# Performance work log

Hardware: AMD Instinct MI355X
Metric: run time of the kernel (lower is better)

Reference implementation:

```python
import jax, jax.numpy as jnp
import numpy as np

D_MODEL, N_HEADS, D_HEAD = 1024, 16, 64
IGNORE = -1e5

def setup_inputs() -> dict:
    key = jax.random.key(0)
    ks = jax.random.split(key, 5)
    std = 0.02
    return {
        "resid_pre": jax.random.normal(ks[0], (4, 2048, D_MODEL), dtype=jnp.float32),
        "W_Q": jax.random.normal(ks[1], (N_HEADS, D_MODEL, D_HEAD), dtype=jnp.float32) * std,
        "W_K": jax.random.normal(ks[2], (N_HEADS, D_MODEL, D_HEAD), dtype=jnp.float32) * std,
        "W_V": jax.random.normal(ks[3], (N_HEADS, D_MODEL, D_HEAD), dtype=jnp.float32) * std,
        "W_O": jax.random.normal(ks[4], (N_HEADS, D_HEAD, D_MODEL), dtype=jnp.float32) * std,
        "b_Q": jnp.zeros((N_HEADS, D_HEAD), dtype=jnp.float32),
        "b_K": jnp.zeros((N_HEADS, D_HEAD), dtype=jnp.float32),
        "b_V": jnp.zeros((N_HEADS, D_HEAD), dtype=jnp.float32),
        "b_O": jnp.zeros((D_MODEL,), dtype=jnp.float32),
    }

def reference(resid_pre, W_Q, W_K, W_V, W_O, b_Q, b_K, b_V, b_O):
    # q/k/v: [batch, posn, n_heads, d_head]
    q = jnp.einsum("hmd,bsm->bshd", W_Q, resid_pre) + b_Q
    k = jnp.einsum("hmd,bsm->bshd", W_K, resid_pre) + b_K
    v = jnp.einsum("hmd,bsm->bshd", W_V, resid_pre) + b_V
    # scores: [batch, n_heads, posn_q, posn_k]
    scores = jnp.einsum("bqhd,bkhd->bhqk", q, k) / jnp.sqrt(jnp.float32(D_HEAD))
    S = resid_pre.shape[1]
    causal = jnp.tril(jnp.ones((S, S), dtype=bool))  # keep where True
    scores = jnp.where(causal, scores, jnp.float32(IGNORE))
    probs = jax.nn.softmax(scores, axis=-1)
    z = jnp.einsum("bhqk,bkhd->bqhd", probs, v)  # [batch, posn_q, n_heads, d_head]
    # project each head to d_model and sum over heads, then add b_O
    attn_out = jnp.einsum("hdm,bqhd->bqm", W_O, z) + b_O
    return attn_out
```

## Files before the change

kernel.cpp:

```cpp
#include <hip/hip_runtime.h>

typedef __bf16 bf16;
typedef __attribute__((ext_vector_type(8))) __bf16 bf16x8;
typedef __attribute__((ext_vector_type(4))) float f32x4;

__device__ __forceinline__ void gload_lds16(const void* g, void* l) {
  __builtin_amdgcn_global_load_lds(
      (const __attribute__((address_space(1))) unsigned int*)(g),
      (__attribute__((address_space(3))) unsigned int*)(l),
      16, 0, 0);
}

__device__ __forceinline__ float exp2_hw(float x) {
  float r; asm("v_exp_f32 %0, %1" : "=v"(r) : "v"(x)); return r;
}
__device__ __forceinline__ unsigned cvtpk_bf16(float a, float b) {
  unsigned r; asm("v_cvt_pk_bf16_f32 %0, %1, %2" : "=v"(r) : "v"(a), "v"(b)); return r;
}

#define QSCALE 0.1803368867f

__global__ __launch_bounds__(256) void pack_all(const float* __restrict__ x,
                                                const float* __restrict__ WQ, const float* __restrict__ WK,
                                                const float* __restrict__ WV,
                                                const float* __restrict__ bQ, const float* __restrict__ bK,
                                                const float* __restrict__ bV,
                                                bf16* __restrict__ Xb, bf16* __restrict__ Wt,
                                                float* __restrict__ biaso) {
  __shared__ float tile[64][65];
  int bid = blockIdx.x;
  int t = threadIdx.x;
  if (bid < 4096) {
    int i = (bid * 256 + t) * 8;
    float4 a = *(const float4*)(x + i);
    float4 b = *(const float4*)(x + i + 4);
    bf16x8 v;
    v[0] = (bf16)a.x; v[1] = (bf16)a.y; v[2] = (bf16)a.z; v[3] = (bf16)a.w;
    v[4] = (bf16)b.x; v[5] = (bf16)b.y; v[6] = (bf16)b.z; v[7] = (bf16)b.w;
    *(bf16x8*)(Xb + i) = v;
  } else if (bid < 4864) {
    int wb = bid - 4096;
    int p = wb >> 8, h = (wb >> 4) & 15, k0 = (wb & 15) * 64;
    const float* src = (p == 0 ? WQ : p == 1 ? WK : WV) + h * 65536;
    float scl = (p == 0) ? QSCALE : 1.0f;
    int c = t & 63, r4 = t >> 6;
#pragma unroll
    for (int rr = 0; rr < 16; ++rr) {
      int k = r4 + rr * 4;
      tile[k][c] = src[(k0 + k) * 64 + c];
    }
    __syncthreads();
#pragma unroll
    for (int rr = 0; rr < 16; ++rr) {
      int d = r4 + rr * 4;
      Wt[(p * 1024 + h * 64 + d) * 1024 + k0 + c] = (bf16)(tile[c][d] * scl);
    }
  } else {
    int i = (bid - 4864) * 256 + t;
    if (i < 3072) {
      int p = i >> 10, j = i & 1023;
      float v = (p == 0 ? bQ : p == 1 ? bK : bV)[j];
      biaso[i] = (p == 0) ? v * QSCALE : v;
    }
  }
}

__global__ __launch_bounds__(256) void pack_wo(const float* __restrict__ WO, bf16* __restrict__ Wt) {
  int bid = blockIdx.x;
  int r0 = (bid >> 4) * 64, c0 = (bid & 15) * 64;
  __shared__ float tile[64][65];
  int t = threadIdx.x, c = t & 63, r4 = t >> 6;
#pragma unroll
  for (int rr = 0; rr < 16; ++rr) {
    int r = r4 + rr * 4;
    tile[r][c] = WO[(r0 + r) * 1024 + c0 + c];
  }
  __syncthreads();
#pragma unroll
  for (int rr = 0; rr < 16; ++rr) {
    int m = r4 + rr * 4;
    Wt[(c0 + m) * 1024 + r0 + c] = (bf16)tile[c][m];
  }
}

template <int OUTF32>
__global__ __launch_bounds__(512, 2) void gemm_bt(const bf16* __restrict__ A, const bf16* __restrict__ Bt,
                                                  const float* __restrict__ bias, void* __restrict__ Cv,
                                                  int M, int N, int K) {
  __shared__ bf16 As[256 * 64];
  __shared__ bf16 Bs[128 * 64];
  int tid = threadIdx.x;
  int wv = tid >> 6, ln = tid & 63, lr = ln & 15, lh = ln >> 4;
  int wr = wv >> 1, wc = wv & 1;
  int row0 = blockIdx.y * 256, col0 = blockIdx.x * 128;
  int ss = (ln & 7) ^ (ln >> 3);
  const char* ga = (const char*)(A + (long)(row0 + wv * 32 + (ln >> 3)) * K) + ss * 16;
  const char* gb = (const char*)(Bt + (long)(col0 + wv * 16 + (ln >> 3)) * K) + ss * 16;
  long rowskip = (long)8 * K * 2;
  f32x4 acc[4][4] = {};
  for (int k0 = 0; k0 < K; k0 += 64) {
#pragma unroll
    for (int i = 0; i < 4; ++i)
      gload_lds16(ga + (long)k0 * 2 + i * rowskip, (char*)As + (wv * 32 + i * 8) * 128);
#pragma unroll
    for (int i = 0; i < 2; ++i)
      gload_lds16(gb + (long)k0 * 2 + i * rowskip, (char*)Bs + (wv * 16 + i * 8) * 128);
    __syncthreads();
    bf16x8 af[4][2], bfr[4][2];
#pragma unroll
    for (int mi = 0; mi < 4; ++mi)
#pragma unroll
      for (int ks = 0; ks < 2; ++ks) {
        int row = wr * 64 + mi * 16 + lr;
        int o = row * 128 + (((ks * 4 + lh) ^ (row & 7)) << 4);
        af[mi][ks] = *(const bf16x8*)((const char*)As + o);
      }
#pragma unroll
    for (int ni = 0; ni < 4; ++ni)
#pragma unroll
      for (int ks = 0; ks < 2; ++ks) {
        int row = wc * 64 + ni * 16 + lr;
        int o = row * 128 + (((ks * 4 + lh) ^ (row & 7)) << 4);
        bfr[ni][ks] = *(const bf16x8*)((const char*)Bs + o);
      }
    __builtin_amdgcn_s_setprio(1);
#pragma unroll
    for (int ks = 0; ks < 2; ++ks)
#pragma unroll
      for (int mi = 0; mi < 4; ++mi)
#pragma unroll
        for (int ni = 0; ni < 4; ++ni)
          acc[mi][ni] = __builtin_amdgcn_mfma_f32_16x16x32_bf16(af[mi][ks], bfr[ni][ks], acc[mi][ni], 0, 0, 0);
    __builtin_amdgcn_s_setprio(0);
    __syncthreads();
  }
#pragma unroll
  for (int mi = 0; mi < 4; ++mi) {
    int row = row0 + wr * 64 + mi * 16 + lh * 4;
#pragma unroll
    for (int ni = 0; ni < 4; ++ni) {
      int col = col0 + wc * 64 + ni * 16 + lr;
      float bvv = bias[col];
#pragma unroll
      for (int r = 0; r < 4; ++r) {
        float v = acc[mi][ni][r] + bvv;
        if (OUTF32) ((float*)Cv)[(long)(row + r) * N + col] = v;
        else        ((bf16*)Cv)[(long)(row + r) * N + col] = (bf16)v;
      }
    }
  }
}

__global__ __launch_bounds__(256, 2) void flash(const bf16* __restrict__ Qkv, bf16* __restrict__ Z) {
  __shared__ bf16 Vt[2][64 * 64];
  __shared__ unsigned char Pl[4][4096];
  const float MASKV = -144269.5041f;
  int bid = blockIdx.x;
  int pair = bid >> 6;
  int bh = (bid & 7) * 8 + ((bid >> 3) & 7);
  int b = bh >> 4, h = bh & 15;
  int tid = threadIdx.x;
  int wv = tid >> 6, ln = tid & 63, lr = ln & 15, lh = ln >> 4;
  const bf16* Qg = Qkv + (long)b * 2048 * 3072 + h * 64;
  const bf16* Kg = Qg + 1024;
  const bf16* Vg = Qg + 2048;
  int vs0 = (tid >> 3) * 2, vd0 = (tid & 7) * 8;
  char* pw = (char*)Pl[wv];

  bf16x8 v0, v1;
  auto loadV = [&](int kvrow0) {
    v0 = *(const bf16x8*)(Vg + (long)(kvrow0 + vs0) * 3072 + vd0);
    v1 = *(const bf16x8*)(Vg + (long)(kvrow0 + vs0 + 1) * 3072 + vd0);
  };
  auto writeV = [&](bf16* vd) {
#pragma unroll
    for (int j = 0; j < 8; ++j) {
      int d = vd0 + j;
      int o = (d * 128 + vs0 * 2) ^ ((((d & 7) ^ (d >> 3)) & 7) << 4);
      unsigned int pk = (unsigned int)__builtin_bit_cast(unsigned short, (bf16)v0[j])
                      | ((unsigned int)__builtin_bit_cast(unsigned short, (bf16)v1[j]) << 16);
      *(unsigned int*)((char*)vd + o) = pk;
    }
  };

#pragma unroll 1
  for (int half = 0; half < 2; ++half) {
    int qt = half ? 15 - pair : pair;
    int q0 = qt * 128;
    int nt = 2 * (qt + 1);
    loadV(0);
    bf16x8 bq[2][2];
#pragma unroll
    for (int mi = 0; mi < 2; ++mi)
#pragma unroll
      for (int ks = 0; ks < 2; ++ks)
        bq[mi][ks] = *(const bf16x8*)(Qg + (long)(q0 + wv * 32 + mi * 16 + lr) * 3072 + ks * 32 + lh * 8);
    writeV(Vt[0]);
    __syncthreads();

    f32x4 oa[4][2] = {};
    float m_st[2], l_st[2];
    m_st[0] = m_st[1] = -1e30f;
    l_st[0] = l_st[1] = 0.f;

    int cur = 0;
    for (int t = 0; t < nt; ++t) {
      int kv0 = t * 64;
      bool more = (t + 1 < nt);
      bf16x8 kf[4][2];
#pragma unroll
      for (int n = 0; n < 4; ++n)
#pragma unroll
        for (int ks = 0; ks < 2; ++ks)
          kf[n][ks] = *(const bf16x8*)(Kg + (long)(kv0 + n * 16 + lr) * 3072 + ks * 32 + lh * 8);
      if (more) loadV(kv0 + 64);
      f32x4 sc[2][4];
      __builtin_amdgcn_s_setprio(1);
#pragma unroll
      for (int mi = 0; mi < 2; ++mi)
#pragma unroll
        for (int n = 0; n < 4; ++n) {
          f32x4 zacc = {0.f, 0.f, 0.f, 0.f};
          zacc = __builtin_amdgcn_mfma_f32_16x16x32_bf16(kf[n][0], bq[mi][0], zacc, 0, 0, 0);
          zacc = __builtin_amdgcn_mfma_f32_16x16x32_bf16(kf[n][1], bq[mi][1], zacc, 0, 0, 0);
          sc[mi][n] = zacc;
        }
      __builtin_amdgcn_s_setprio(0);
      if (kv0 + 63 > q0) {
#pragma unroll
        for (int mi = 0; mi < 2; ++mi) {
          int qrow = q0 + wv * 32 + mi * 16 + lr;
#pragma unroll
          for (int n = 0; n < 4; ++n) {
            int kvb = kv0 + n * 16 + lh * 4;
#pragma unroll
            for (int r = 0; r < 4; ++r)
              if (kvb + r > qrow) sc[mi][n][r] = MASKV;
          }
        }
      }
#pragma unroll
      for (int mi = 0; mi < 2; ++mi) {
        float mx = sc[mi][0][0];
#pragma unroll
        for (int n = 0; n < 4; ++n)
#pragma unroll
          for (int r = 0; r < 4; ++r) mx = fmaxf(mx, sc[mi][n][r]);
        mx = fmaxf(mx, __shfl_xor(mx, 16));
        mx = fmaxf(mx, __shfl_xor(mx, 32));
        if (!__all(mx <= m_st[mi] + 8.0f)) {
          float mn = fmaxf(m_st[mi], mx);
          float resc = exp2_hw(m_st[mi] - mn);
          m_st[mi] = mn;
          l_st[mi] *= resc;
#pragma unroll
          for (int n2 = 0; n2 < 4; ++n2)
#pragma unroll
            for (int r = 0; r < 4; ++r) oa[n2][mi][r] *= resc;
        }
        float s = 0.f;
#pragma unroll
        for (int n = 0; n < 4; ++n)
#pragma unroll
          for (int r = 0; r < 4; ++r) {
            float p = exp2_hw(sc[mi][n][r] - m_st[mi]);
            sc[mi][n][r] = p;
            s += p;
          }
        s += __shfl_xor(s, 16);
        s += __shfl_xor(s, 32);
        l_st[mi] += s;
      }
#pragma unroll
      for (int mi = 0; mi < 2; ++mi) {
        int row = mi * 16 + lr;
#pragma unroll
        for (int n = 0; n < 4; ++n) {
          int addr = row * 128 + ((n * 32 + lh * 8) ^ ((row & 7) << 4));
          uint2 val = { cvtpk_bf16(sc[mi][n][0], sc[mi][n][1]),
                        cvtpk_bf16(sc[mi][n][2], sc[mi][n][3]) };
          *(uint2*)(pw + addr) = val;
        }
      }
      if (more) writeV(Vt[cur ^ 1]);
      bf16x8 pa[2][2];
#pragma unroll
      for (int mi = 0; mi < 2; ++mi)
#pragma unroll
        for (int ks = 0; ks < 2; ++ks) {
          int row = mi * 16 + lr;
          int o = row * 128 + (((ks * 4 + lh) ^ (row & 7)) << 4);
          pa[mi][ks] = *(const bf16x8*)(pw + o);
        }
      __builtin_amdgcn_s_setprio(1);
#pragma unroll
      for (int n2 = 0; n2 < 4; ++n2) {
        int row = n2 * 16 + lr;
        int o0 = row * 128 + ((((0 + lh) ^ (row & 7) ^ ((row >> 3) & 7)) & 7) << 4);
        int o1 = row * 128 + ((((4 + lh) ^ (row & 7) ^ ((row >> 3) & 7)) & 7) << 4);
        bf16x8 vf0 = *(const bf16x8*)((const char*)Vt[cur] + o0);
        bf16x8 vf1 = *(const bf16x8*)((const char*)Vt[cur] + o1);
#pragma unroll
        for (int mi = 0; mi < 2; ++mi) {
          oa[n2][mi] = __builtin_amdgcn_mfma_f32_16x16x32_bf16(vf0, pa[mi][0], oa[n2][mi], 0, 0, 0);
          oa[n2][mi] = __builtin_amdgcn_mfma_f32_16x16x32_bf16(vf1, pa[mi][1], oa[n2][mi], 0, 0, 0);
        }
      }
      __builtin_amdgcn_s_setprio(0);
      __syncthreads();
      cur ^= 1;
    }
#pragma unroll
    for (int mi = 0; mi < 2; ++mi) {
      float inv = 1.0f / l_st[mi];
      int q = q0 + wv * 32 + mi * 16 + lr;
      bf16* zb = Z + ((long)b * 2048 + q) * 1024 + h * 64 + lh * 4;
#pragma unroll
      for (int n2 = 0; n2 < 4; ++n2) {
        uint2 o2 = { cvtpk_bf16(oa[n2][mi][0] * inv, oa[n2][mi][1] * inv),
                     cvtpk_bf16(oa[n2][mi][2] * inv, oa[n2][mi][3] * inv) };
        *(uint2*)(zb + n2 * 16) = o2;
      }
    }
  }
}

extern "C" void kernel_launch(void* const* d_in, const int* in_sizes, int n_in,
                              void* d_out, int out_size, void* d_ws, size_t ws_size,
                              hipStream_t stream) {
  const float* resid = (const float*)d_in[0];
  const float* WQ = (const float*)d_in[1];
  const float* WK = (const float*)d_in[2];
  const float* WV = (const float*)d_in[3];
  const float* WO = (const float*)d_in[4];
  const float* bQ = (const float*)d_in[5];
  const float* bK = (const float*)d_in[6];
  const float* bV = (const float*)d_in[7];
  const float* bO = (const float*)d_in[8];
  char* ws = (char*)d_ws;
  bf16*  Xb      = (bf16*)ws;
  bf16*  Z       = (bf16*)ws;
  bf16*  Wqkv    = (bf16*)(ws + 16777216);
  bf16*  Wot     = (bf16*)(ws + 16777216);
  float* biasqkv = (float*)(ws + 23068672);
  bf16*  QKVo    = (bf16*)(ws + 23085056);

  pack_all<<<4876, 256, 0, stream>>>(resid, WQ, WK, WV, bQ, bK, bV, Xb, Wqkv, biasqkv);
  gemm_bt<0><<<dim3(24, 32), 512, 0, stream>>>(Xb, Wqkv, biasqkv, QKVo, 8192, 3072, 1024);
  pack_wo<<<256, 256, 0, stream>>>(WO, Wot);
  flash<<<512, 256, 0, stream>>>(QKVo, Z);
  gemm_bt<1><<<dim3(8, 32), 512, 0, stream>>>(Z, Wot, bO, d_out, 8192, 1024, 1024);
}
```

Measured before the change: 298.0 us.

## Shrink GEMM tiles to 128x128 and double-buffer K fragments in flash loop

The GEMM kernel moves from 512-thread 256x128 tiles to 256-thread 128x128 tiles, with twice as many blocks in the grid. This trades per-block reuse for more blocks and possibly better occupancy. The flash attention loop is unrolled by two with ping-pong K register buffers, so the next tile's K fragments load while the current tile's softmax and PV run, hiding global load latency. The cost is higher register pressure and a loop that assumes an even tile count, which holds since nt = 2*(qt+1).

```diff
diff --git a/kernel.cpp b/kernel.cpp
--- a/kernel.cpp
+++ b/kernel.cpp
@@ -84,27 +84,26 @@
 }
 
 template <int OUTF32>
-__global__ __launch_bounds__(512, 2) void gemm_bt(const bf16* __restrict__ A, const bf16* __restrict__ Bt,
+__global__ __launch_bounds__(256, 2) void gemm_bt(const bf16* __restrict__ A, const bf16* __restrict__ Bt,
                                                   const float* __restrict__ bias, void* __restrict__ Cv,
                                                   int M, int N, int K) {
-  __shared__ bf16 As[256 * 64];
+  __shared__ bf16 As[128 * 64];
   __shared__ bf16 Bs[128 * 64];
   int tid = threadIdx.x;
   int wv = tid >> 6, ln = tid & 63, lr = ln & 15, lh = ln >> 4;
   int wr = wv >> 1, wc = wv & 1;
-  int row0 = blockIdx.y * 256, col0 = blockIdx.x * 128;
+  int row0 = blockIdx.y * 128, col0 = blockIdx.x * 128;
   int ss = (ln & 7) ^ (ln >> 3);
   const char* ga = (const char*)(A + (long)(row0 + wv * 32 + (ln >> 3)) * K) + ss * 16;
-  const char* gb = (const char*)(Bt + (long)(col0 + wv * 16 + (ln >> 3)) * K) + ss * 16;
+  const char* gb = (const char*)(Bt + (long)(col0 + wv * 32 + (ln >> 3)) * K) + ss * 16;
   long rowskip = (long)8 * K * 2;
   f32x4 acc[4][4] = {};
   for (int k0 = 0; k0 < K; k0 += 64) {
 #pragma unroll
-    for (int i = 0; i < 4; ++i)
+    for (int i = 0; i < 4; ++i) {
       gload_lds16(ga + (long)k0 * 2 + i * rowskip, (char*)As + (wv * 32 + i * 8) * 128);
-#pragma unroll
-    for (int i = 0; i < 2; ++i)
-      gload_lds16(gb + (long)k0 * 2 + i * rowskip, (char*)Bs + (wv * 16 + i * 8) * 128);
+      gload_lds16(gb + (long)k0 * 2 + i * rowskip, (char*)Bs + (wv * 32 + i * 8) * 128);
+    }
     __syncthreads();
     bf16x8 af[4][2], bfr[4][2];
 #pragma unroll
@@ -183,6 +182,114 @@
     }
   };
 
+#define FLASH_STEP(T, KF, KFN) do {                                                   \
+    int kv0 = (T) * 64;                                                               \
+    bool more = (T) + 1 < nt;                                                         \
+    if (more) loadV(kv0 + 64);                                                        \
+    f32x4 sc[2][4];                                                                   \
+    __builtin_amdgcn_s_setprio(1);                                                    \
+    _Pragma("unroll")                                                                 \
+    for (int mi = 0; mi < 2; ++mi)                                                    \
+      _Pragma("unroll")                                                               \
+      for (int n = 0; n < 4; ++n) {                                                   \
+        f32x4 zacc = {0.f, 0.f, 0.f, 0.f};                                            \
+        zacc = __builtin_amdgcn_mfma_f32_16x16x32_bf16(KF[n][0], bq[mi][0], zacc, 0, 0, 0); \
+        zacc = __builtin_amdgcn_mfma_f32_16x16x32_bf16(KF[n][1], bq[mi][1], zacc, 0, 0, 0); \
+        sc[mi][n] = zacc;                                                             \
+      }                                                                               \
+    __builtin_amdgcn_s_setprio(0);                                                    \
+    if (more) {                          \
+      _Pragma("unroll")                                                               \
+      for (int n = 0; n < 4; ++n)                                                     \
+        _Pragma("unroll")                                                             \
+        for (int ks = 0; ks < 2; ++ks)                                                \
+          KFN[n][ks] = *(const bf16x8*)(Kg + (long)(kv0 + 64 + n * 16 + lr) * 3072 + ks * 32 + lh * 8); \
+    }                                                                                 \
+    if (kv0 + 63 > q0) {                                                              \
+      _Pragma("unroll")                                                               \
+      for (int mi = 0; mi < 2; ++mi) {                                                \
+        int qrow = q0 + wv * 32 + mi * 16 + lr;                                       \
+        _Pragma("unroll")                                                             \
+        for (int n = 0; n < 4; ++n) {                                                 \
+          int kvb = kv0 + n * 16 + lh * 4;                                            \
+          _Pragma("unroll")                                                           \
+          for (int r = 0; r < 4; ++r)                                                 \
+            if (kvb + r > qrow) sc[mi][n][r] = MASKV;                                 \
+        }                                                                             \
+      }                                                                               \
+    }                                                                                 \
+    _Pragma("unroll")                                                                 \
+    for (int mi = 0; mi < 2; ++mi) {                                                  \
+      float mx = sc[mi][0][0];                                                        \
+      _Pragma("unroll")                                                               \
+      for (int n = 0; n < 4; ++n)                                                     \
+        _Pragma("unroll")                                                             \
+        for (int r = 0; r < 4; ++r) mx = fmaxf(mx, sc[mi][n][r]);                     \
+      mx = fmaxf(mx, __shfl_xor(mx, 16));                                             \
+      mx = fmaxf(mx, __shfl_xor(mx, 32));                                             \
+      if (!__all(mx <= m_st[mi] + 8.0f)) {                             \
+        float mn = fmaxf(m_st[mi], mx);                                               \
+        float resc = exp2_hw(m_st[mi] - mn);                                          \
+        m_st[mi] = mn;                                                                \
+        l_st[mi] *= resc;                                                             \
+        _Pragma("unroll")                                                             \
+        for (int n2 = 0; n2 < 4; ++n2)                                                \
+          _Pragma("unroll")                                                           \
+          for (int r = 0; r < 4; ++r) oa[n2][mi][r] *= resc;                          \
+      }                                                                               \
+      float s = 0.f;                                                                  \
+      _Pragma("unroll")                                                               \
+      for (int n = 0; n < 4; ++n)                                                     \
+        _Pragma("unroll")                                                             \
+        for (int r = 0; r < 4; ++r) {                                                 \
+          float p = exp2_hw(sc[mi][n][r] - m_st[mi]);                                 \
+          sc[mi][n][r] = p;                                                           \
+          s += p;                                                                     \
+        }                                                                             \
+      s += __shfl_xor(s, 16);                                                         \
+      s += __shfl_xor(s, 32);                                                         \
+      l_st[mi] += s;                                                                  \
+    }                                                                                 \
+    _Pragma("unroll")                                                                 \
+    for (int mi = 0; mi < 2; ++mi) {                                                  \
+      int row = mi * 16 + lr;                                                         \
+      _Pragma("unroll")                                                               \
+      for (int n = 0; n < 4; ++n) {                                                   \
+        int addr = row * 128 + ((n * 32 + lh * 8) ^ ((row & 7) << 4));                \
+        uint2 val = { cvtpk_bf16(sc[mi][n][0], sc[mi][n][1]),                         \
+                      cvtpk_bf16(sc[mi][n][2], sc[mi][n][3]) };                       \
+        *(uint2*)(pw + addr) = val;                                                   \
+      }                                                                               \
+    }                                                                                 \
+    if (more) writeV(Vt[cur ^ 1]);                                                    \
+    bf16x8 pa[2][2];                                                                  \
+    _Pragma("unroll")                                                                 \
+    for (int mi = 0; mi < 2; ++mi)                                                    \
+      _Pragma("unroll")                                                               \
+      for (int ks = 0; ks < 2; ++ks) {                                                \
+        int row = mi * 16 + lr;                                                       \
+        int o = row * 128 + (((ks * 4 + lh) ^ (row & 7)) << 4);                       \
+        pa[mi][ks] = *(const bf16x8*)(pw + o);                                        \
+      }                                                                               \
+    __builtin_amdgcn_s_setprio(1);                                                    \
+    _Pragma("unroll")                                                                 \
+    for (int n2 = 0; n2 < 4; ++n2) {                                                  \
+      int row = n2 * 16 + lr;                                                         \
+      int o0 = row * 128 + ((((0 + lh) ^ (row & 7) ^ ((row >> 3) & 7)) & 7) << 4);    \
+      int o1 = row * 128 + ((((4 + lh) ^ (row & 7) ^ ((row >> 3) & 7)) & 7) << 4);    \
+      bf16x8 vf0 = *(const bf16x8*)((const char*)Vt[cur] + o0);                       \
+      bf16x8 vf1 = *(const bf16x8*)((const char*)Vt[cur] + o1);                       \
+      _Pragma("unroll")                                                               \
+      for (int mi = 0; mi < 2; ++mi) {                                                \
+        oa[n2][mi] = __builtin_amdgcn_mfma_f32_16x16x32_bf16(vf0, pa[mi][0], oa[n2][mi], 0, 0, 0); \
+        oa[n2][mi] = __builtin_amdgcn_mfma_f32_16x16x32_bf16(vf1, pa[mi][1], oa[n2][mi], 0, 0, 0); \
+      }                                                                               \
+    }                                                                                 \
+    __builtin_amdgcn_s_setprio(0);                                                    \
+    __syncthreads();                                                                  \
+    cur ^= 1;                                                                         \
+  } while (0)
+
 #pragma unroll 1
   for (int half = 0; half < 2; ++half) {
     int qt = half ? 15 - pair : pair;
@@ -195,6 +302,12 @@
 #pragma unroll
       for (int ks = 0; ks < 2; ++ks)
         bq[mi][ks] = *(const bf16x8*)(Qg + (long)(q0 + wv * 32 + mi * 16 + lr) * 3072 + ks * 32 + lh * 8);
+    bf16x8 kfA[4][2], kfB[4][2];
+#pragma unroll
+    for (int n = 0; n < 4; ++n)
+#pragma unroll
+      for (int ks = 0; ks < 2; ++ks)
+        kfA[n][ks] = *(const bf16x8*)(Kg + (long)(n * 16 + lr) * 3072 + ks * 32 + lh * 8);
     writeV(Vt[0]);
     __syncthreads();
 
@@ -204,111 +317,10 @@
     l_st[0] = l_st[1] = 0.f;
 
     int cur = 0;
-    for (int t = 0; t < nt; ++t) {
-      int kv0 = t * 64;
-      bool more = (t + 1 < nt);
-      bf16x8 kf[4][2];
-#pragma unroll
-      for (int n = 0; n < 4; ++n)
-#pragma unroll
-        for (int ks = 0; ks < 2; ++ks)
-          kf[n][ks] = *(const bf16x8*)(Kg + (long)(kv0 + n * 16 + lr) * 3072 + ks * 32 + lh * 8);
-      if (more) loadV(kv0 + 64);
-      f32x4 sc[2][4];
-      __builtin_amdgcn_s_setprio(1);
-#pragma unroll
-      for (int mi = 0; mi < 2; ++mi)
-#pragma unroll
-        for (int n = 0; n < 4; ++n) {
-          f32x4 zacc = {0.f, 0.f, 0.f, 0.f};
-          zacc = __builtin_amdgcn_mfma_f32_16x16x32_bf16(kf[n][0], bq[mi][0], zacc, 0, 0, 0);
-          zacc = __builtin_amdgcn_mfma_f32_16x16x32_bf16(kf[n][1], bq[mi][1], zacc, 0, 0, 0);
-          sc[mi][n] = zacc;
-        }
-      __builtin_amdgcn_s_setprio(0);
-      if (kv0 + 63 > q0) {
-#pragma unroll
-        for (int mi = 0; mi < 2; ++mi) {
-          int qrow = q0 + wv * 32 + mi * 16 + lr;
-#pragma unroll
-          for (int n = 0; n < 4; ++n) {
-            int kvb = kv0 + n * 16 + lh * 4;
-#pragma unroll
-            for (int r = 0; r < 4; ++r)
-              if (kvb + r > qrow) sc[mi][n][r] = MASKV;
-          }
-        }
-      }
-#pragma unroll
-      for (int mi = 0; mi < 2; ++mi) {
-        float mx = sc[mi][0][0];
-#pragma unroll
-        for (int n = 0; n < 4; ++n)
-#pragma unroll
-          for (int r = 0; r < 4; ++r) mx = fmaxf(mx, sc[mi][n][r]);
-        mx = fmaxf(mx, __shfl_xor(mx, 16));
-        mx = fmaxf(mx, __shfl_xor(mx, 32));
-        if (!__all(mx <= m_st[mi] + 8.0f)) {
-          float mn = fmaxf(m_st[mi], mx);
-          float resc = exp2_hw(m_st[mi] - mn);
-          m_st[mi] = mn;
-          l_st[mi] *= resc;
-#pragma unroll
-          for (int n2 = 0; n2 < 4; ++n2)
-#pragma unroll
-            for (int r = 0; r < 4; ++r) oa[n2][mi][r] *= resc;
-        }
-        float s = 0.f;
-#pragma unroll
-        for (int n = 0; n < 4; ++n)
-#pragma unroll
-          for (int r = 0; r < 4; ++r) {
-            float p = exp2_hw(sc[mi][n][r] - m_st[mi]);
-            sc[mi][n][r] = p;
-            s += p;
-          }
-        s += __shfl_xor(s, 16);
-        s += __shfl_xor(s, 32);
-        l_st[mi] += s;
-      }
-#pragma unroll
-      for (int mi = 0; mi < 2; ++mi) {
-        int row = mi * 16 + lr;
-#pragma unroll
-        for (int n = 0; n < 4; ++n) {
-          int addr = row * 128 + ((n * 32 + lh * 8) ^ ((row & 7) << 4));
-          uint2 val = { cvtpk_bf16(sc[mi][n][0], sc[mi][n][1]),
-                        cvtpk_bf16(sc[mi][n][2], sc[mi][n][3]) };
-          *(uint2*)(pw + addr) = val;
-        }
-      }
-      if (more) writeV(Vt[cur ^ 1]);
-      bf16x8 pa[2][2];
-#pragma unroll
-      for (int mi = 0; mi < 2; ++mi)
-#pragma unroll
-        for (int ks = 0; ks < 2; ++ks) {
-          int row = mi * 16 + lr;
-          int o = row * 128 + (((ks * 4 + lh) ^ (row & 7)) << 4);
-          pa[mi][ks] = *(const bf16x8*)(pw + o);
-        }
-      __builtin_amdgcn_s_setprio(1);
-#pragma unroll
-      for (int n2 = 0; n2 < 4; ++n2) {
-        int row = n2 * 16 + lr;
-        int o0 = row * 128 + ((((0 + lh) ^ (row & 7) ^ ((row >> 3) & 7)) & 7) << 4);
-        int o1 = row * 128 + ((((4 + lh) ^ (row & 7) ^ ((row >> 3) & 7)) & 7) << 4);
-        bf16x8 vf0 = *(const bf16x8*)((const char*)Vt[cur] + o0);
-        bf16x8 vf1 = *(const bf16x8*)((const char*)Vt[cur] + o1);
-#pragma unroll
-        for (int mi = 0; mi < 2; ++mi) {
-          oa[n2][mi] = __builtin_amdgcn_mfma_f32_16x16x32_bf16(vf0, pa[mi][0], oa[n2][mi], 0, 0, 0);
-          oa[n2][mi] = __builtin_amdgcn_mfma_f32_16x16x32_bf16(vf1, pa[mi][1], oa[n2][mi], 0, 0, 0);
-        }
-      }
-      __builtin_amdgcn_s_setprio(0);
-      __syncthreads();
-      cur ^= 1;
+#pragma unroll 1
+    for (int t = 0; t < nt; t += 2) {
+      FLASH_STEP(t, kfA, kfB);
+      FLASH_STEP(t + 1, kfB, kfA);
     }
 #pragma unroll
     for (int mi = 0; mi < 2; ++mi) {
@@ -323,6 +335,7 @@
       }
     }
   }
+#undef FLASH_STEP
 }
 
 extern "C" void kernel_launch(void* const* d_in, const int* in_sizes, int n_in,
@@ -346,8 +359,8 @@
   bf16*  QKVo    = (bf16*)(ws + 23085056);
 
   pack_all<<<4876, 256, 0, stream>>>(resid, WQ, WK, WV, bQ, bK, bV, Xb, Wqkv, biasqkv);
-  gemm_bt<0><<<dim3(24, 32), 512, 0, stream>>>(Xb, Wqkv, biasqkv, QKVo, 8192, 3072, 1024);
+  gemm_bt<0><<<dim3(24, 64), 256, 0, stream>>>(Xb, Wqkv, biasqkv, QKVo, 8192, 3072, 1024);
   pack_wo<<<256, 256, 0, stream>>>(WO, Wot);
   flash<<<512, 256, 0, stream>>>(QKVo, Z);
-  gemm_bt<1><<<dim3(8, 32), 512, 0, stream>>>(Z, Wot, bO, d_out, 8192, 1024, 1024);
-}
+  gemm_bt<1><<<dim3(8, 64), 256, 0, stream>>>(Z, Wot, bO, d_out, 8192, 1024, 1024);
+}
```

After: 271.5 us. 1.1x faster.
